# Kernel optimization log

Hardware: AMD Instinct MI355X
Metric: run time of the kernel (lower is better)

Reference implementation:

```python
import jax, jax.numpy as jnp
import numpy as np

MARGIN = 0.3
N_CLASSES = 256
N_SAMPLES = 32
D = 2048

def setup_inputs() -> dict:
    key = jax.random.key(0)
    k1, k2 = jax.random.split(key)
    embeddings = jax.random.normal(k1, (2 * N_CLASSES * N_SAMPLES, D), dtype=jnp.float32)
    target = jax.random.randint(k2, (2 * N_CLASSES * N_SAMPLES,), 0, N_CLASSES, dtype=jnp.int64 if jax.config.jax_enable_x64 else jnp.int32)
    return {"embeddings": embeddings, "target": target, "margin": MARGIN, "n_classes": N_CLASSES, "n_samples": N_SAMPLES}

def reference(embeddings, target, margin, n_classes, n_samples):
    # target is unused by the original forward (kept for signature fidelity).
    d = embeddings.shape[-1]
    # [C, 2, S, D]: slot 0 = positives, slot 1 = negatives per class
    e = embeddings.reshape(n_classes, 2, n_samples, d)
    pos, neg = e[:, 0], e[:, 1]                      # [C, S, D]
    anchor = pos.mean(axis=1, keepdims=True)          # [C, 1, D]
    ap = jnp.sqrt(jnp.sum((pos - anchor) ** 2, axis=-1))           # [C, S]
    neg_d2 = jnp.sum((neg - anchor) ** 2, axis=-1)                 # [C, S]
    # hardest negative: min squared distance to anchor -> its sqrt is an_distance
    an = jnp.sqrt(jnp.min(neg_d2, axis=1, keepdims=True))          # [C, 1]
    losses = jnp.sum(jax.nn.relu(ap - an + margin) ** 2, axis=1)   # [C]
    return losses.mean()
```

## Files before the change

kernel.cpp:

```cpp
#include <hip/hip_runtime.h>

#define NCLS 256
#define NSMP 32
#define DIM  2048
#define DV   (DIM / 4)
#define BLK  512
#define NWAVE (BLK / 64)

__global__ __launch_bounds__(BLK, 2)
void ccl_kernel(const float* __restrict__ emb,
                const float* __restrict__ margin_p,
                float* __restrict__ out) {
    const int c    = blockIdx.x;
    const int tid  = threadIdx.x;
    const int wave = tid >> 6;
    const int lane = tid & 63;

    __shared__ float pp[NWAVE][NSMP];
    __shared__ float pn[NWAVE][NSMP];

    const float4* pos = (const float4*)(emb + (size_t)c * 2 * NSMP * DIM);
    const float4* neg = pos + (size_t)NSMP * DV;

    float4 x[NSMP];
    #pragma unroll
    for (int i = 0; i < NSMP; ++i) x[i] = pos[(size_t)i * DV + tid];

    float4 a = make_float4(0.f, 0.f, 0.f, 0.f);
    #pragma unroll
    for (int i = 0; i < NSMP; ++i) {
        a.x += x[i].x; a.y += x[i].y; a.z += x[i].z; a.w += x[i].w;
    }
    const float inv = 1.0f / (float)NSMP;
    a.x *= inv; a.y *= inv; a.z *= inv; a.w *= inv;

    #pragma unroll
    for (int i = 0; i < NSMP; ++i) {
        float dx = x[i].x - a.x, dy = x[i].y - a.y;
        float dz = x[i].z - a.z, dw = x[i].w - a.w;
        float p  = dx * dx + dy * dy + dz * dz + dw * dw;
        #pragma unroll
        for (int off = 32; off >= 1; off >>= 1) p += __shfl_xor(p, off, 64);
        if (lane == 0) pp[wave][i] = p;
    }

    #pragma unroll
    for (int i = 0; i < NSMP; ++i) {
        float4 n = neg[(size_t)i * DV + tid];
        float dx = n.x - a.x, dy = n.y - a.y;
        float dz = n.z - a.z, dw = n.w - a.w;
        float p  = dx * dx + dy * dy + dz * dz + dw * dw;
        #pragma unroll
        for (int off = 32; off >= 1; off >>= 1) p += __shfl_xor(p, off, 64);
        if (lane == 0) pn[wave][i] = p;
    }
    __syncthreads();

    if (wave == 0) {
        float d2p = 0.f, d2n = 0.f;
        if (lane < NSMP) {
            #pragma unroll
            for (int w = 0; w < NWAVE; ++w) { d2p += pp[w][lane]; d2n += pn[w][lane]; }
        } else {
            d2n = 3.4e38f;
        }

        float nd = d2n;
        #pragma unroll
        for (int off = 32; off >= 1; off >>= 1) nd = fminf(nd, __shfl_xor(nd, off, 64));
        const float an = sqrtf(nd);
        const float margin = margin_p[0];

        float l = 0.f;
        if (lane < NSMP) {
            float ap = sqrtf(d2p);
            float v  = fmaxf(ap - an + margin, 0.f);
            l = v * v;
        }
        #pragma unroll
        for (int off = 32; off >= 1; off >>= 1) l += __shfl_xor(l, off, 64);
        if (lane == 0) atomicAdd(out, l * (1.0f / (float)NCLS));
    }
}

extern "C" void kernel_launch(void* const* d_in, const int* in_sizes, int n_in,
                              void* d_out, int out_size, void* d_ws, size_t ws_size,
                              hipStream_t stream) {
    const float* emb    = (const float*)d_in[0];
    const float* margin = (const float*)d_in[2];
    float* out = (float*)d_out;

    hipMemsetAsync(out, 0, sizeof(float), stream);
    ccl_kernel<<<NCLS, BLK, 0, stream>>>(emb, margin, out);
}
```

Before: 211.0 us.

## Replace per-sample wave shuffles with shared-memory transpose reduction and prefetch negatives

Each thread now writes its per-sample partial squared distances into a padded shared-memory array. Sixteen threads per sample then sum each row, which replaces 32 six-step cross-wave shuffle reductions for each of the positive and negative sets. Negative rows are also loaded ahead through an 8-deep register ring so they overlap with the positive-side work. The cost is about 66KB of shared memory and extra syncthreads, which may lower occupancy below the two blocks per CU that launch_bounds asks for.

```diff
diff --git a/kernel.cpp b/kernel.cpp
--- a/kernel.cpp
+++ b/kernel.cpp
@@ -5,19 +5,19 @@
 #define DIM  2048
 #define DV   (DIM / 4)
 #define BLK  512
-#define NWAVE (BLK / 64)
+#define ROWS 520
+#define PF   8
 
 __global__ __launch_bounds__(BLK, 2)
 void ccl_kernel(const float* __restrict__ emb,
                 const float* __restrict__ margin_p,
                 float* __restrict__ out) {
-    const int c    = blockIdx.x;
-    const int tid  = threadIdx.x;
-    const int wave = tid >> 6;
-    const int lane = tid & 63;
+    const int c   = blockIdx.x;
+    const int tid = threadIdx.x;
 
-    __shared__ float pp[NWAVE][NSMP];
-    __shared__ float pn[NWAVE][NSMP];
+    __shared__ float part[NSMP * ROWS];
+    __shared__ float d2p[NSMP];
+    __shared__ float d2n[NSMP];
 
     const float4* pos = (const float4*)(emb + (size_t)c * 2 * NSMP * DIM);
     const float4* neg = pos + (size_t)NSMP * DV;
@@ -34,52 +34,72 @@
     const float inv = 1.0f / (float)NSMP;
     a.x *= inv; a.y *= inv; a.z *= inv; a.w *= inv;
 
+    float4 nb[PF];
+    #pragma unroll
+    for (int j = 0; j < PF; ++j) nb[j] = neg[(size_t)j * DV + tid];
+
     #pragma unroll
     for (int i = 0; i < NSMP; ++i) {
         float dx = x[i].x - a.x, dy = x[i].y - a.y;
         float dz = x[i].z - a.z, dw = x[i].w - a.w;
-        float p  = dx * dx + dy * dy + dz * dz + dw * dw;
+        part[i * ROWS + tid] = dx * dx + dy * dy + dz * dz + dw * dw;
+    }
+    __syncthreads();
+
+    const int s   = tid >> 4;
+    const int c16 = tid & 15;
+    {
+        float sum = 0.f;
         #pragma unroll
-        for (int off = 32; off >= 1; off >>= 1) p += __shfl_xor(p, off, 64);
-        if (lane == 0) pp[wave][i] = p;
+        for (int k = 0; k < 8; ++k) {
+            float4 v = *(const float4*)&part[s * ROWS + c16 * 4 + k * 64];
+            sum += v.x + v.y + v.z + v.w;
+        }
+        #pragma unroll
+        for (int off = 8; off >= 1; off >>= 1) sum += __shfl_xor(sum, off, 64);
+        if (c16 == 0) d2p[s] = sum;
     }
+    __syncthreads();
 
     #pragma unroll
     for (int i = 0; i < NSMP; ++i) {
-        float4 n = neg[(size_t)i * DV + tid];
+        float4 n = nb[i & (PF - 1)];
+        if (i + PF < NSMP) nb[i & (PF - 1)] = neg[(size_t)(i + PF) * DV + tid];
         float dx = n.x - a.x, dy = n.y - a.y;
         float dz = n.z - a.z, dw = n.w - a.w;
-        float p  = dx * dx + dy * dy + dz * dz + dw * dw;
-        #pragma unroll
-        for (int off = 32; off >= 1; off >>= 1) p += __shfl_xor(p, off, 64);
-        if (lane == 0) pn[wave][i] = p;
+        part[i * ROWS + tid] = dx * dx + dy * dy + dz * dz + dw * dw;
     }
     __syncthreads();
 
-    if (wave == 0) {
-        float d2p = 0.f, d2n = 0.f;
-        if (lane < NSMP) {
-            #pragma unroll
-            for (int w = 0; w < NWAVE; ++w) { d2p += pp[w][lane]; d2n += pn[w][lane]; }
-        } else {
-            d2n = 3.4e38f;
+    {
+        float sum = 0.f;
+        #pragma unroll
+        for (int k = 0; k < 8; ++k) {
+            float4 v = *(const float4*)&part[s * ROWS + c16 * 4 + k * 64];
+            sum += v.x + v.y + v.z + v.w;
         }
+        #pragma unroll
+        for (int off = 8; off >= 1; off >>= 1) sum += __shfl_xor(sum, off, 64);
+        if (c16 == 0) d2n[s] = sum;
+    }
+    __syncthreads();
 
-        float nd = d2n;
+    if (tid < 64) {
+        float nd = (tid < NSMP) ? d2n[tid] : 3.4e38f;
         #pragma unroll
         for (int off = 32; off >= 1; off >>= 1) nd = fminf(nd, __shfl_xor(nd, off, 64));
         const float an = sqrtf(nd);
         const float margin = margin_p[0];
 
         float l = 0.f;
-        if (lane < NSMP) {
-            float ap = sqrtf(d2p);
+        if (tid < NSMP) {
+            float ap = sqrtf(d2p[tid]);
             float v  = fmaxf(ap - an + margin, 0.f);
             l = v * v;
         }
         #pragma unroll
         for (int off = 32; off >= 1; off >>= 1) l += __shfl_xor(l, off, 64);
-        if (lane == 0) atomicAdd(out, l * (1.0f / (float)NCLS));
+        if (tid == 0) atomicAdd(out, l * (1.0f / (float)NCLS));
     }
 }
 
```

New measurement: 198.0 us, median of 2. 6.2% less time.
